# Performance work log

Hardware: AMD Instinct MI355X
Metric: run time of the kernel (lower is better)

The kernel has to match this reference:

```python
import jax, jax.numpy as jnp
import numpy as np

S = 512   # grid side (data_patch_size)
BS = 8    # batch size


def _make_faces(h, w):
    idx = np.arange(h * w).reshape(h, w)
    v0 = idx[:-1, :-1].ravel(); v1 = idx[:-1, 1:].ravel()
    v2 = idx[1:, :-1].ravel(); v3 = idx[1:, 1:].ravel()
    t1 = np.stack([v0, v1, v2], axis=1)
    t2 = np.stack([v1, v3, v2], axis=1)
    return np.concatenate([t1, t2], axis=0).astype(np.int32)


def _vertex_tri_maps(faces, n_verts):
    # Vectorized equivalent of vertex_tri_maps: ragged vertex->triangle lists,
    # padded to max degree c, weight 1.0 for real entries, 0.0 for padding.
    F = faces.shape[0]
    vid = faces.ravel()
    fid = np.repeat(np.arange(F, dtype=np.int32), 3)
    order = np.argsort(vid, kind='stable')
    vid_s = vid[order]; fid_s = fid[order]
    counts = np.bincount(vid_s, minlength=n_verts)
    starts = np.concatenate([[0], np.cumsum(counts)[:-1]])
    pos = np.arange(len(vid_s)) - starts[vid_s]
    c = int(counts.max())  # 6 for a grid mesh
    idx = np.zeros((n_verts, c), dtype=np.int32)
    wt = np.zeros((n_verts, c), dtype=np.float32)
    idx[vid_s, pos] = fid_s
    wt[vid_s, pos] = 1.0
    return idx, wt[None, :, :, None]  # weights: (1, V, c, 1)


def setup_inputs() -> dict:
    key = jax.random.key(0)
    faces = _make_faces(S, S)
    n_verts = S * S
    vti, vtw = _vertex_tri_maps(faces, n_verts)
    vrt = jax.random.normal(key, (BS, n_verts, 3), dtype=jnp.float32)
    return {
        "vrt": vrt,
        "vert_tri_weights": jnp.asarray(vtw),
        "faces": jnp.asarray(faces),
        "vert_tri_indices": jnp.asarray(vti),
    }


def _l2norm(x, eps=1e-12):
    # torch F.normalize(p=2): x / max(||x||, eps)
    n = jnp.linalg.norm(x, axis=-1, keepdims=True)
    return x / jnp.maximum(n, eps)


def reference(vrt, vert_tri_weights, faces, vert_tri_indices):
    # face normals: (bs, F, 3)
    v1 = vrt[:, faces[:, 1]] - vrt[:, faces[:, 0]]
    v2 = vrt[:, faces[:, 2]] - vrt[:, faces[:, 0]]
    fn = _l2norm(jnp.cross(v1, v2))
    # gather per-vertex triangle normals: (bs, V, c, 3)
    fn_group = fn[:, vert_tri_indices]
    # weighted sum over triangle group, then normalize: (bs, V, 3)
    vn = (fn_group * vert_tri_weights).sum(axis=-2)
    return _l2norm(vn)
```

## Files before the change

kernel.cpp:

```cpp
#include <hip/hip_runtime.h>
#include <math.h>


typedef float f3 __attribute__((ext_vector_type(3)));

__device__ __forceinline__ f3 load_pt(const float* __restrict__ base,
                                      int S, int rr, int cc) {
    return *reinterpret_cast<const f3*>(base + (size_t)(rr * S + cc) * 3);
}

__device__ __forceinline__ void accum_face(float w, f3 e1, f3 e2, f3& s) {
    float nx = e1.y * e2.z - e1.z * e2.y;
    float ny = e1.z * e2.x - e1.x * e2.z;
    float nz = e1.x * e2.y - e1.y * e2.x;
    float d  = nx * nx + ny * ny + nz * nz;
    float inv = (d > 0.0f) ? rsqrtf(d) : 0.0f;
    inv *= w;
    s.x = fmaf(nx, inv, s.x);
    s.y = fmaf(ny, inv, s.y);
    s.z = fmaf(nz, inv, s.z);
}

__global__ __launch_bounds__(256) void vertex_normals_stencil(
    const float* __restrict__ vrt,
    float*       __restrict__ out,
    int S)
{
    int c = blockIdx.x * blockDim.x + threadIdx.x;
    int r = blockIdx.y;
    int b = blockIdx.z;
    if (c >= S) return;
    int n_verts = S * S;

    int rm = (r > 0) ? r - 1 : 0;
    int rp = (r < S - 1) ? r + 1 : S - 1;
    int cm = (c > 0) ? c - 1 : 0;
    int cp = (c < S - 1) ? c + 1 : S - 1;

    const float* base = vrt + (size_t)b * n_verts * 3;

    f3 A  = load_pt(base, S, r,  c);
    f3 L  = load_pt(base, S, r,  cm);
    f3 R  = load_pt(base, S, r,  cp);
    f3 U  = load_pt(base, S, rm, c);
    f3 D  = load_pt(base, S, rp, c);
    f3 UR = load_pt(base, S, rm, cp);
    f3 DL = load_pt(base, S, rp, cm);

    float w_dn = (r < S - 1) ? 1.0f : 0.0f;
    float w_up = (r > 0)     ? 1.0f : 0.0f;
    float w_rt = (c < S - 1) ? 1.0f : 0.0f;
    float w_lt = (c > 0)     ? 1.0f : 0.0f;

    f3 s; s.x = 0.f; s.y = 0.f; s.z = 0.f;

    accum_face(w_dn * w_rt, R - A,  D - A,  s);
    accum_face(w_dn * w_lt, A - L,  DL - L, s);
    accum_face(w_up * w_rt, UR - U, A - U,  s);
    accum_face(w_dn * w_lt, D - A,  DL - A, s);
    accum_face(w_up * w_lt, A - U,  L - U,  s);
    accum_face(w_up * w_rt, R - UR, A - UR, s);

    float nrm = sqrtf(s.x * s.x + s.y * s.y + s.z * s.z);
    float inv = 1.0f / fmaxf(nrm, 1e-12f);

    f3 o;
    o.x = s.x * inv;
    o.y = s.y * inv;
    o.z = s.z * inv;
    *reinterpret_cast<f3*>(out + ((size_t)b * n_verts + (size_t)r * S + c) * 3) = o;
}

extern "C" void kernel_launch(void* const* d_in, const int* in_sizes, int n_in,
                              void* d_out, int out_size, void* d_ws, size_t ws_size,
                              hipStream_t stream) {
    const float* vrt = (const float*)d_in[0];
    float*       out = (float*)d_out;

    int F = in_sizes[2] / 3;
    int S = 1 + (int)(sqrt((double)(F / 2)) + 0.5);
    int n_verts = S * S;
    int BS = in_sizes[0] / (3 * n_verts);

    dim3 grid((S + 255) / 256, S, BS);
    vertex_normals_stencil<<<grid, 256, 0, stream>>>(vrt, out, S);
}
```

Before: 96.44 us.

## Process four rows per thread, reusing loaded neighbor rows in registers

Each thread now computes normals for four consecutive rows in one column. It loads a 6x3 window of neighbor points into registers once instead of issuing seven loads per vertex. This cuts redundant global and L2 load traffic, but raises register pressure and reduces the number of blocks in the grid.

```diff
diff --git a/kernel.cpp b/kernel.cpp
--- a/kernel.cpp
+++ b/kernel.cpp
@@ -3,6 +3,8 @@
 
 
 typedef float f3 __attribute__((ext_vector_type(3)));
+
+#define RPT 4
 
 __device__ __forceinline__ f3 load_pt(const float* __restrict__ base,
                                       int S, int rr, int cc) {
@@ -26,49 +28,60 @@
     float*       __restrict__ out,
     int S)
 {
-    int c = blockIdx.x * blockDim.x + threadIdx.x;
-    int r = blockIdx.y;
-    int b = blockIdx.z;
+    int c  = blockIdx.x * blockDim.x + threadIdx.x;
+    int r0 = blockIdx.y * RPT;
+    int b  = blockIdx.z;
     if (c >= S) return;
     int n_verts = S * S;
 
-    int rm = (r > 0) ? r - 1 : 0;
-    int rp = (r < S - 1) ? r + 1 : S - 1;
     int cm = (c > 0) ? c - 1 : 0;
     int cp = (c < S - 1) ? c + 1 : S - 1;
+    float w_rt = (c < S - 1) ? 1.0f : 0.0f;
+    float w_lt = (c > 0)     ? 1.0f : 0.0f;
 
     const float* base = vrt + (size_t)b * n_verts * 3;
 
-    f3 A  = load_pt(base, S, r,  c);
-    f3 L  = load_pt(base, S, r,  cm);
-    f3 R  = load_pt(base, S, r,  cp);
-    f3 U  = load_pt(base, S, rm, c);
-    f3 D  = load_pt(base, S, rp, c);
-    f3 UR = load_pt(base, S, rm, cp);
-    f3 DL = load_pt(base, S, rp, cm);
+    f3 P[RPT + 2][3];
+    #pragma unroll
+    for (int i = 0; i < RPT + 2; ++i) {
+        int rr = r0 - 1 + i;
+        rr = (rr < 0) ? 0 : ((rr > S - 1) ? S - 1 : rr);
+        P[i][0] = load_pt(base, S, rr, cm);
+        P[i][1] = load_pt(base, S, rr, c);
+        P[i][2] = load_pt(base, S, rr, cp);
+    }
 
-    float w_dn = (r < S - 1) ? 1.0f : 0.0f;
-    float w_up = (r > 0)     ? 1.0f : 0.0f;
-    float w_rt = (c < S - 1) ? 1.0f : 0.0f;
-    float w_lt = (c > 0)     ? 1.0f : 0.0f;
+    float* ob = out + ((size_t)b * n_verts + (size_t)r0 * S + c) * 3;
 
-    f3 s; s.x = 0.f; s.y = 0.f; s.z = 0.f;
+    #pragma unroll
+    for (int k = 0; k < RPT; ++k) {
+        int r = r0 + k;
+        if (r >= S) break;
+        float w_dn = (r < S - 1) ? 1.0f : 0.0f;
+        float w_up = (r > 0)     ? 1.0f : 0.0f;
 
-    accum_face(w_dn * w_rt, R - A,  D - A,  s);
-    accum_face(w_dn * w_lt, A - L,  DL - L, s);
-    accum_face(w_up * w_rt, UR - U, A - U,  s);
-    accum_face(w_dn * w_lt, D - A,  DL - A, s);
-    accum_face(w_up * w_lt, A - U,  L - U,  s);
-    accum_face(w_up * w_rt, R - UR, A - UR, s);
+        f3 U  = P[k][1],     UR = P[k][2];
+        f3 L  = P[k + 1][0], A  = P[k + 1][1], R = P[k + 1][2];
+        f3 DL = P[k + 2][0], D  = P[k + 2][1];
 
-    float nrm = sqrtf(s.x * s.x + s.y * s.y + s.z * s.z);
-    float inv = 1.0f / fmaxf(nrm, 1e-12f);
+        f3 s; s.x = 0.f; s.y = 0.f; s.z = 0.f;
 
-    f3 o;
-    o.x = s.x * inv;
-    o.y = s.y * inv;
-    o.z = s.z * inv;
-    *reinterpret_cast<f3*>(out + ((size_t)b * n_verts + (size_t)r * S + c) * 3) = o;
+        accum_face(w_dn * w_rt, R - A,  D - A,  s);
+        accum_face(w_dn * w_lt, A - L,  DL - L, s);
+        accum_face(w_up * w_rt, UR - U, A - U,  s);
+        accum_face(w_dn * w_lt, D - A,  DL - A, s);
+        accum_face(w_up * w_lt, A - U,  L - U,  s);
+        accum_face(w_up * w_rt, R - UR, A - UR, s);
+
+        float nrm = sqrtf(s.x * s.x + s.y * s.y + s.z * s.z);
+        float inv = 1.0f / fmaxf(nrm, 1e-12f);
+
+        f3 o;
+        o.x = s.x * inv;
+        o.y = s.y * inv;
+        o.z = s.z * inv;
+        *reinterpret_cast<f3*>(ob + (size_t)k * S * 3) = o;
+    }
 }
 
 extern "C" void kernel_launch(void* const* d_in, const int* in_sizes, int n_in,
@@ -82,6 +95,6 @@
     int n_verts = S * S;
     int BS = in_sizes[0] / (3 * n_verts);
 
-    dim3 grid((S + 255) / 256, S, BS);
+    dim3 grid((S + 255) / 256, (S + RPT - 1) / RPT, BS);
     vertex_normals_stencil<<<grid, 256, 0, stream>>>(vrt, out, S);
 }
```

Result: faster. 93.58 us (-3.0%).
